# Kernel tuning notes

Measured on AMD Instinct MI355X. Metric: run time of the kernel, lower is better.

Reference implementation:

```python
import math
import jax, jax.numpy as jnp
import numpy as np

D_MODEL = 512
MAX_SEQ = 512
NUM_OUT = 16
H = 1  # num_heads


def _pos_encoding(d_model, seq_len):
    # sinusoidal PE, then flipped along the sequence axis (ReversedPositionalEncoding)
    pos = jnp.arange(seq_len, dtype=jnp.float32)[:, None]
    i = jnp.arange(0, d_model, 2, dtype=jnp.float32)
    ang = pos * jnp.exp(i * (-(math.log(10000.0) / d_model)))  # [S, d/2]
    pe = jnp.stack([jnp.sin(ang), jnp.cos(ang)], axis=-1).reshape(seq_len, d_model)
    return pe[::-1]


def _layernorm(x, w, b, eps=1e-5):
    m = jnp.mean(x, axis=-1, keepdims=True)
    v = jnp.mean(jnp.square(x - m), axis=-1, keepdims=True)
    return (x - m) / jnp.sqrt(v + eps) * w + b


def setup_inputs() -> dict:
    key = jax.random.key(0)
    ks = jax.random.split(key, 8)
    B = 128
    latents = jax.random.normal(ks[0], (B, D_MODEL, MAX_SEQ), dtype=jnp.float32)
    query_mask = jnp.ones((B, NUM_OUT), dtype=jnp.float32)
    query = 0.02 * jax.random.normal(ks[1], (NUM_OUT, D_MODEL), dtype=jnp.float32)
    return {
        "latents": latents,
        "query_mask": query_mask,
        "query": query,
        "ln_lat_w": jnp.ones((D_MODEL,), jnp.float32),
        "ln_lat_b": jnp.zeros((D_MODEL,), jnp.float32),
        "ln_q_w": jnp.ones((D_MODEL,), jnp.float32),
        "ln_q_b": jnp.zeros((D_MODEL,), jnp.float32),
        "Wq": 0.02 * jax.random.normal(ks[2], (D_MODEL, D_MODEL), jnp.float32),
        "bq": jnp.zeros((D_MODEL,), jnp.float32),
        "Wk": 0.02 * jax.random.normal(ks[3], (D_MODEL, D_MODEL), jnp.float32),
        "bk": jnp.zeros((D_MODEL,), jnp.float32),
        "Wv": 0.02 * jax.random.normal(ks[4], (D_MODEL, D_MODEL), jnp.float32),
        "bv": jnp.zeros((D_MODEL,), jnp.float32),
        "Wo": 0.02 * jax.random.normal(ks[5], (1, D_MODEL), jnp.float32),
        "bo": jnp.zeros((1,), jnp.float32),
    }


def reference(latents, query_mask, query, ln_lat_w, ln_lat_b, ln_q_w, ln_q_b,
              Wq, bq, Wk, bk, Wv, bv, Wo, bo):
    B, _, N = latents.shape  # latents: [B, d_model, N]
    scale = math.sqrt(D_MODEL)
    Dh = D_MODEL // H

    # cross-attention mask: query_mask [B,Nq] x all-ones latent mask [B,N]
    mask = jnp.einsum('bq,bk->bqk', query_mask, jnp.ones((B, N), latents.dtype))

    x = jnp.swapaxes(latents, 1, 2) * scale           # [B, N, d]
    x = x + _pos_encoding(D_MODEL, MAX_SEQ)[-N:]      # reversed PE, last N positions
    # dropout is identity in eval mode
    x = _layernorm(x, ln_lat_w, ln_lat_b)

    q = _layernorm(query * scale, ln_q_w, ln_q_b)     # [Nq, d]
    q = jnp.broadcast_to(q[None], (B, NUM_OUT, D_MODEL))

    qh = (q @ Wq.T + bq).reshape(B, NUM_OUT, H, Dh)
    kh = (x @ Wk.T + bk).reshape(B, N, H, Dh)
    vh = (x @ Wv.T + bv).reshape(B, N, H, Dh)

    scores = jnp.einsum('bqhd,bkhd->bhqk', qh, kh) / math.sqrt(Dh)
    scores = jnp.where(mask[:, None] == 0, -1e9, scores)
    attn_weights = jax.nn.softmax(scores, axis=-1)    # [B, H, Nq, N]

    attn = jnp.einsum('bhqk,bkhd->bqhd', attn_weights, vh).reshape(B, NUM_OUT, H * Dh)
    wipe = jnp.all(mask == 0, axis=2, keepdims=True)  # [B, Nq, 1]
    attn = jnp.where(wipe, 0.0, attn)

    logits = attn @ Wo.T + bo                         # [B, Nq, 1]
    return logits, attn_weights
```

## Files before the change

### kernel.cpp

```cpp
#include <hip/hip_runtime.h>
#include <math.h>

#define DM 512
#define NQ 16
#define NG (NQ + 1)

__device__ __forceinline__ float wave_reduce_sum(float v) {
    #pragma unroll
    for (int off = 32; off > 0; off >>= 1) v += __shfl_xor(v, off, 64);
    return v;
}
__device__ __forceinline__ float wave_reduce_max(float v) {
    #pragma unroll
    for (int off = 32; off > 0; off >>= 1) v = fmaxf(v, __shfl_xor(v, off, 64));
    return v;
}

__global__ void k1_setup(const float* __restrict__ Wk, const float* __restrict__ Wv,
                         const float* __restrict__ query,
                         const float* __restrict__ ln_q_w, const float* __restrict__ ln_q_b,
                         float* __restrict__ PET, float* __restrict__ WkT,
                         float* __restrict__ WvT, float* __restrict__ q_ln, int N) {
    __shared__ float tile[64][65];
    int bx = blockIdx.x;
    int lane = threadIdx.x & 63;
    int w = threadIdx.x >> 6;

    if (bx < 128) {
        int ntile = bx & 7, jg = bx >> 3;
        int n = ntile * 64 + lane;
        float p = (float)(N - 1 - n);
        const float c = -logf(10000.f) / (float)DM;
        int jbase = jg * 16 + w * 4;
        #pragma unroll
        for (int u = 0; u < 4; ++u) {
            int j = jbase + u;
            float wj = expf((float)(2 * j) * c);
            float ang = p * wj;
            PET[(size_t)(2 * j) * N + n] = sinf(ang);
            PET[(size_t)(2 * j + 1) * N + n] = cosf(ang);
        }
    } else if (bx < 256) {
        int t = bx - 128;
        const float* W = (t >> 6) ? Wv : Wk;
        float* WT = (t >> 6) ? WvT : WkT;
        int tl = t & 63;
        int te = tl >> 3, td = tl & 7;
        #pragma unroll
        for (int i = 0; i < 16; ++i) {
            int el = w * 16 + i;
            tile[el][lane] = W[(size_t)(te * 64 + el) * DM + td * 64 + lane];
        }
        __syncthreads();
        #pragma unroll
        for (int i = 0; i < 16; ++i) {
            int dl = w * 16 + i;
            WT[(size_t)(td * 64 + dl) * DM + te * 64 + lane] = tile[lane][dl];
        }
    } else {
        const float scale = 22.627416997969522f;
        for (int qi = 0; qi < 4; ++qi) {
            int q = w * 4 + qi;
            float vals[8], s = 0.f, s2 = 0.f;
            #pragma unroll
            for (int i = 0; i < 8; ++i) {
                float x = query[q * DM + i * 64 + lane] * scale;
                vals[i] = x; s += x; s2 += x * x;
            }
            s = wave_reduce_sum(s); s2 = wave_reduce_sum(s2);
            float m = s * (1.f / DM);
            float var = s2 * (1.f / DM) - m * m;
            float rstd = rsqrtf(var + 1e-5f);
            #pragma unroll
            for (int i = 0; i < 8; ++i) {
                int d = i * 64 + lane;
                q_ln[q * DM + d] = (vals[i] - m) * rstd * ln_q_w[d] + ln_q_b[d];
            }
        }
    }
}

__global__ void k2_qh(const float* __restrict__ q_ln, const float* __restrict__ Wq,
                      const float* __restrict__ bq, float* __restrict__ qh) {
    int idx = blockIdx.x * 4 + (threadIdx.x >> 6);
    int lane = threadIdx.x & 63;
    int q = idx >> 9, e = idx & 511;
    const float4* wr = (const float4*)(Wq + (size_t)e * DM);
    const float4* xr = (const float4*)(q_ln + (size_t)q * DM);
    float4 w0 = wr[lane * 2], w1 = wr[lane * 2 + 1];
    float4 x0 = xr[lane * 2], x1 = xr[lane * 2 + 1];
    float s = w0.x * x0.x + w0.y * x0.y + w0.z * x0.z + w0.w * x0.w
            + w1.x * x1.x + w1.y * x1.y + w1.z * x1.z + w1.w * x1.w;
    s = wave_reduce_sum(s);
    if (lane == 0) qh[q * DM + e] = s + bq[e];
}

__global__ void k3_qt(const float* __restrict__ qh, const float* __restrict__ WkT,
                      const float* __restrict__ Wo, const float* __restrict__ WvT,
                      const float* __restrict__ lnw,
                      float* __restrict__ qt, float* __restrict__ A,
                      float* __restrict__ wvout) {
    int idx = blockIdx.x * 4 + (threadIdx.x >> 6);
    int lane = threadIdx.x & 63;
    int g = idx >> 9, d = idx & 511;
    const float4* wr;
    const float4* xr;
    if (g < NQ) {
        wr = (const float4*)(WkT + (size_t)d * DM);
        xr = (const float4*)(qh + (size_t)g * DM);
    } else {
        wr = (const float4*)(WvT + (size_t)d * DM);
        xr = (const float4*)Wo;
    }
    float4 w0 = wr[lane * 2], w1 = wr[lane * 2 + 1];
    float4 x0 = xr[lane * 2], x1 = xr[lane * 2 + 1];
    float s = w0.x * x0.x + w0.y * x0.y + w0.z * x0.z + w0.w * x0.w
            + w1.x * x1.x + w1.y * x1.y + w1.z * x1.z + w1.w * x1.w;
    s = wave_reduce_sum(s);
    if (lane == 0) {
        if (g < NQ) qt[g * DM + d] = s;
        else wvout[d] = s;
        A[g * DM + d] = s * lnw[d];
    }
}

__global__ void k4_pea(const float* __restrict__ A, const float* __restrict__ PET,
                       const float* __restrict__ qt, const float* __restrict__ qh,
                       const float* __restrict__ wv, const float* __restrict__ lnb,
                       const float* __restrict__ bk, const float* __restrict__ Wo,
                       const float* __restrict__ bv,
                       float* __restrict__ peA, float* __restrict__ peS,
                       float* __restrict__ peQ, float* __restrict__ consts, int N) {
    __shared__ float red[4][64];
    int bx = blockIdx.x;
    int lane = threadIdx.x & 63;
    int w = threadIdx.x >> 6;

    if (bx < 152) {
        int g = bx >> 3, ntile = bx & 7;
        int n = ntile * 64 + lane;
        int d0 = w * 128;
        float acc = 0.f;
        if (g < NG) {
            for (int i = 0; i < 128; ++i) {
                int d = d0 + i;
                acc = fmaf(A[(size_t)g * DM + d], PET[(size_t)d * N + n], acc);
            }
        } else if (g == NG) {
            for (int i = 0; i < 128; ++i) acc += PET[(size_t)(d0 + i) * N + n];
        } else {
            for (int i = 0; i < 128; ++i) {
                float v = PET[(size_t)(d0 + i) * N + n];
                acc = fmaf(v, v, acc);
            }
        }
        red[w][lane] = acc;
        __syncthreads();
        if (w != 0) return;
        float tot = red[0][lane] + red[1][lane] + red[2][lane] + red[3][lane];
        if (g < NG) peA[(size_t)g * N + n] = tot;
        else if (g == NG) peS[n] = tot;
        else peQ[n] = tot;
    } else {
        int t = (bx - 152) * 4 + w;
        if (t > NQ) return;
        if (t < NQ) {
            float sa = 0.f, sc = 0.f, qb = 0.f;
            #pragma unroll
            for (int i = 0; i < 8; ++i) {
                int d = i * 64 + lane;
                sa += A[t * DM + d];
                sc = fmaf(qt[t * DM + d], lnb[d], sc);
                qb = fmaf(qh[t * DM + d], bk[d], qb);
            }
            sa = wave_reduce_sum(sa);
            sc = wave_reduce_sum(sc);
            qb = wave_reduce_sum(qb);
            if (lane == 0) { consts[t] = sa; consts[16 + t] = sc + qb; }
        } else {
            float sa = 0.f, cv = 0.f, bvo = 0.f;
            #pragma unroll
            for (int i = 0; i < 8; ++i) {
                int d = i * 64 + lane;
                sa += A[NQ * DM + d];
                cv = fmaf(wv[d], lnb[d], cv);
                bvo = fmaf(Wo[d], bv[d], bvo);
            }
            sa = wave_reduce_sum(sa);
            cv = wave_reduce_sum(cv);
            bvo = wave_reduce_sum(bvo);
            if (lane == 0) { consts[32] = sa; consts[33] = cv + bvo; }
        }
    }
}

__launch_bounds__(256, 4)
__global__ void main_kernel(const float* __restrict__ latents,
                            const float* __restrict__ PET,
                            const float* __restrict__ A,
                            const float* __restrict__ peA,
                            const float* __restrict__ peS,
                            const float* __restrict__ peQ,
                            const float* __restrict__ consts,
                            float* __restrict__ scores,
                            float* __restrict__ vbuf, int N) {
    int b = blockIdx.y;
    int lane = threadIdx.x & 63;
    int wv = threadIdx.x >> 6;
    int n = blockIdx.x * 64 + lane;
    const float scale = 22.627416997969522f;

    int d0 = __builtin_amdgcn_readfirstlane(wv * (DM / 4));
    const float* lat = latents + (size_t)b * DM * N + (size_t)d0 * N + n;
    const float* pet = PET + (size_t)d0 * N + n;

    float acc[NG];
    #pragma unroll
    for (int i = 0; i < NG; ++i) acc[i] = 0.f;
    float S1 = 0.f, S2 = 0.f, Sx = 0.f;

    const int U = 8;
    const int NC = (DM / 4) / U;
    float xb[2][U], pb[2][U];
    #pragma unroll
    for (int u = 0; u < U; ++u) {
        xb[0][u] = __builtin_nontemporal_load(&lat[(size_t)u * N]);
        pb[0][u] = pet[(size_t)u * N];
    }
    int cur = 0;
    for (int c = 0; c < NC; ++c) {
        int nxt = cur ^ 1;
        if (c + 1 < NC) {
            #pragma unroll
            for (int u = 0; u < U; ++u) {
                size_t dd = (size_t)((c + 1) * U + u) * N;
                xb[nxt][u] = __builtin_nontemporal_load(&lat[dd]);
                pb[nxt][u] = pet[dd];
            }
        }
        #pragma unroll
        for (int u = 0; u < U; ++u) {
            float x = xb[cur][u], pe = pb[cur][u];
            S1 += x; S2 = fmaf(x, x, S2); Sx = fmaf(x, pe, Sx);
            int d = d0 + c * U + u;
            #pragma unroll
            for (int q = 0; q < NG; ++q)
                acc[q] = fmaf(A[(size_t)q * DM + d], x, acc[q]);
        }
        cur = nxt;
    }

    __shared__ float red[4][NG + 3][64];
    red[wv][0][lane] = S1;
    red[wv][1][lane] = S2;
    red[wv][2][lane] = Sx;
    #pragma unroll
    for (int i = 0; i < NG; ++i) red[wv][3 + i][lane] = acc[i];
    __syncthreads();
    if (wv != 0) return;

    float tot[NG + 3];
    #pragma unroll
    for (int i = 0; i < NG + 3; ++i)
        tot[i] = red[0][i][lane] + red[1][i][lane] + red[2][i][lane] + red[3][i][lane];

    float s1 = tot[0], s2 = tot[1], sx = tot[2];
    float m = (scale * s1 + peS[n]) * (1.f / DM);
    float ex2 = (scale * scale * s2 + 2.f * scale * sx + peQ[n]) * (1.f / DM);
    float rstd = rsqrtf(ex2 - m * m + 1e-5f);

    float sumAv = consts[32], CvT = consts[33];
    float v = rstd * (scale * tot[3 + NQ] + peA[(size_t)NQ * N + n] - m * sumAv) + CvT;
    vbuf[(size_t)b * N + n] = v;

    const float isd = 0.044194173824159216f;
    #pragma unroll
    for (int q = 0; q < NQ; ++q) {
        float sc = (rstd * (scale * tot[3 + q] + peA[(size_t)q * N + n] - m * consts[q])
                    + consts[16 + q]) * isd;
        scores[((size_t)b * NQ + q) * N + n] = sc;
    }
}

__global__ void softmax_kernel(const float* __restrict__ scores,
                               const float* __restrict__ vbuf,
                               const float* __restrict__ query_mask,
                               const float* __restrict__ bo,
                               float* __restrict__ out_logits,
                               float* __restrict__ out_attn, int N) {
    int r = blockIdx.x * 4 + (threadIdx.x >> 6);
    int b = r >> 4;
    int lane = threadIdx.x & 63;
    float* attn_row = out_attn + (size_t)r * N;
    float qm = query_mask[r];
    if (qm == 0.f) {
        float u = 1.f / (float)N;
        for (int i = 0; i < N / 64; ++i) attn_row[i * 64 + lane] = u;
        if (lane == 0) out_logits[r] = bo[0];
        return;
    }
    const float* srow = scores + (size_t)r * N;
    float sv[8];
    float mx = -1e30f;
    for (int i = 0; i < N / 64; ++i) { sv[i] = srow[i * 64 + lane]; mx = fmaxf(mx, sv[i]); }
    mx = wave_reduce_max(mx);
    float sum = 0.f;
    for (int i = 0; i < N / 64; ++i) { sv[i] = expf(sv[i] - mx); sum += sv[i]; }
    sum = wave_reduce_sum(sum);
    float inv = 1.f / sum;
    const float* vrow = vbuf + (size_t)b * N;
    float lp = 0.f;
    for (int i = 0; i < N / 64; ++i) {
        float w = sv[i] * inv;
        attn_row[i * 64 + lane] = w;
        lp += w * vrow[i * 64 + lane];
    }
    lp = wave_reduce_sum(lp);
    if (lane == 0) out_logits[r] = lp + bo[0];
}

extern "C" void kernel_launch(void* const* d_in, const int* in_sizes, int n_in,
                              void* d_out, int out_size, void* d_ws, size_t ws_size,
                              hipStream_t stream) {
    const float* latents    = (const float*)d_in[0];
    const float* query_mask = (const float*)d_in[1];
    const float* query      = (const float*)d_in[2];
    const float* ln_lat_w   = (const float*)d_in[3];
    const float* ln_lat_b   = (const float*)d_in[4];
    const float* ln_q_w     = (const float*)d_in[5];
    const float* ln_q_b     = (const float*)d_in[6];
    const float* Wq         = (const float*)d_in[7];
    const float* bq         = (const float*)d_in[8];
    const float* Wk         = (const float*)d_in[9];
    const float* bk         = (const float*)d_in[10];
    const float* Wv         = (const float*)d_in[11];
    const float* bv         = (const float*)d_in[12];
    const float* Wo         = (const float*)d_in[13];
    const float* bo         = (const float*)d_in[14];

    int B = in_sizes[1] / NQ;
    int N = in_sizes[0] / (DM * B);

    float* ws = (float*)d_ws;
    size_t off = 0;
    float* PET    = ws + off; off += (size_t)DM * N;
    float* WkT    = ws + off; off += (size_t)DM * DM;
    float* WvT    = ws + off; off += (size_t)DM * DM;
    float* peS    = ws + off; off += N;
    float* peQ    = ws + off; off += N;
    float* q_ln   = ws + off; off += NQ * DM;
    float* qh     = ws + off; off += NQ * DM;
    float* qt     = ws + off; off += NQ * DM;
    float* A      = ws + off; off += NG * DM;
    float* wv     = ws + off; off += DM;
    float* peA    = ws + off; off += (size_t)NG * N;
    float* consts = ws + off; off += 64;
    float* scores = ws + off; off += (size_t)B * NQ * N;
    float* vbuf   = ws + off; off += (size_t)B * N;

    float* out_logits = (float*)d_out;
    float* out_attn   = out_logits + (size_t)B * NQ;

    k1_setup<<<257, 256, 0, stream>>>(Wk, Wv, query, ln_q_w, ln_q_b,
                                      PET, WkT, WvT, q_ln, N);
    k2_qh<<<NQ * DM / 4, 256, 0, stream>>>(q_ln, Wq, bq, qh);
    k3_qt<<<NG * DM / 4, 256, 0, stream>>>(qh, WkT, Wo, WvT, ln_lat_w, qt, A, wv);
    k4_pea<<<157, 256, 0, stream>>>(A, PET, qt, qh, wv, ln_lat_b, bk, Wo, bv,
                                    peA, peS, peQ, consts, N);
    dim3 gmain(N / 64, B);
    main_kernel<<<gmain, 256, 0, stream>>>(latents, PET, A, peA, peS, peQ, consts,
                                           scores, vbuf, N);
    softmax_kernel<<<B * NQ / 4, 256, 0, stream>>>(scores, vbuf, query_mask, bo,
                                                   out_logits, out_attn, N);
}
```

Before: 283.0 us.

## Process two columns per thread with packed FMA and vectorize softmax

The main kernel now has each thread handle two adjacent sequence positions. It uses v_pk_fma_f32 inline asm against a duplicated scalar A coefficient, stored as an extra A2 buffer, to halve the FMA instruction count, and it issues 8-byte vector loads and stores. The grid is halved along N and each wave now covers 128 rows of d. The softmax kernel switches to float4 loads and stores and hardcodes two float4 chunks per lane, which assumes N=512. Each block now streams twice the data, so there are fewer blocks and less parallelism, and register pressure rises.

```diff
diff --git a/kernel.cpp b/kernel.cpp
--- a/kernel.cpp
+++ b/kernel.cpp
@@ -4,6 +4,8 @@
 #define DM 512
 #define NQ 16
 #define NG (NQ + 1)
+
+typedef __attribute__((ext_vector_type(2))) float f32x2;
 
 __device__ __forceinline__ float wave_reduce_sum(float v) {
     #pragma unroll
@@ -99,7 +101,7 @@
                       const float* __restrict__ Wo, const float* __restrict__ WvT,
                       const float* __restrict__ lnw,
                       float* __restrict__ qt, float* __restrict__ A,
-                      float* __restrict__ wvout) {
+                      f32x2* __restrict__ A2, float* __restrict__ wvout) {
     int idx = blockIdx.x * 4 + (threadIdx.x >> 6);
     int lane = threadIdx.x & 63;
     int g = idx >> 9, d = idx & 511;
@@ -120,7 +122,10 @@
     if (lane == 0) {
         if (g < NQ) qt[g * DM + d] = s;
         else wvout[d] = s;
-        A[g * DM + d] = s * lnw[d];
+        float a = s * lnw[d];
+        A[g * DM + d] = a;
+        f32x2 ap; ap.x = a; ap.y = a;
+        A2[g * DM + d] = ap;
     }
 }
 
@@ -197,7 +202,7 @@
 __launch_bounds__(256, 4)
 __global__ void main_kernel(const float* __restrict__ latents,
                             const float* __restrict__ PET,
-                            const float* __restrict__ A,
+                            const unsigned long long* __restrict__ A2,
                             const float* __restrict__ peA,
                             const float* __restrict__ peS,
                             const float* __restrict__ peQ,
@@ -206,26 +211,26 @@
                             float* __restrict__ vbuf, int N) {
     int b = blockIdx.y;
     int lane = threadIdx.x & 63;
-    int wv = threadIdx.x >> 6;
-    int n = blockIdx.x * 64 + lane;
+    int w = threadIdx.x >> 6;
+    int n0 = blockIdx.x * 128 + lane * 2;
     const float scale = 22.627416997969522f;
 
-    int d0 = __builtin_amdgcn_readfirstlane(wv * (DM / 4));
-    const float* lat = latents + (size_t)b * DM * N + (size_t)d0 * N + n;
-    const float* pet = PET + (size_t)d0 * N + n;
-
-    float acc[NG];
-    #pragma unroll
-    for (int i = 0; i < NG; ++i) acc[i] = 0.f;
-    float S1 = 0.f, S2 = 0.f, Sx = 0.f;
-
-    const int U = 8;
-    const int NC = (DM / 4) / U;
-    float xb[2][U], pb[2][U];
+    int d0 = __builtin_amdgcn_readfirstlane(w * 128);
+    const float* latf = latents + (size_t)b * DM * N + (size_t)d0 * N + n0;
+    const float* petf = PET + (size_t)d0 * N + n0;
+
+    f32x2 acc[NG];
+    #pragma unroll
+    for (int i = 0; i < NG; ++i) { acc[i].x = 0.f; acc[i].y = 0.f; }
+    f32x2 S1 = {0.f, 0.f}, S2 = {0.f, 0.f}, Sx = {0.f, 0.f};
+
+    const int U = 4;
+    const int NC = 128 / U;
+    f32x2 xb[2][U], pb[2][U];
     #pragma unroll
     for (int u = 0; u < U; ++u) {
-        xb[0][u] = __builtin_nontemporal_load(&lat[(size_t)u * N]);
-        pb[0][u] = pet[(size_t)u * N];
+        xb[0][u] = __builtin_nontemporal_load((const f32x2*)(latf + (size_t)u * N));
+        pb[0][u] = *(const f32x2*)(petf + (size_t)u * N);
     }
     int cur = 0;
     for (int c = 0; c < NC; ++c) {
@@ -234,51 +239,61 @@
             #pragma unroll
             for (int u = 0; u < U; ++u) {
                 size_t dd = (size_t)((c + 1) * U + u) * N;
-                xb[nxt][u] = __builtin_nontemporal_load(&lat[dd]);
-                pb[nxt][u] = pet[dd];
+                xb[nxt][u] = __builtin_nontemporal_load((const f32x2*)(latf + dd));
+                pb[nxt][u] = *(const f32x2*)(petf + dd);
             }
         }
         #pragma unroll
         for (int u = 0; u < U; ++u) {
-            float x = xb[cur][u], pe = pb[cur][u];
-            S1 += x; S2 = fmaf(x, x, S2); Sx = fmaf(x, pe, Sx);
+            f32x2 x = xb[cur][u], pe = pb[cur][u];
+            S1 += x;
+            S2.x = fmaf(x.x, x.x, S2.x); S2.y = fmaf(x.y, x.y, S2.y);
+            Sx.x = fmaf(x.x, pe.x, Sx.x); Sx.y = fmaf(x.y, pe.y, Sx.y);
             int d = d0 + c * U + u;
             #pragma unroll
-            for (int q = 0; q < NG; ++q)
-                acc[q] = fmaf(A[(size_t)q * DM + d], x, acc[q]);
+            for (int q = 0; q < NG; ++q) {
+                unsigned long long a = A2[(size_t)q * DM + d];
+                asm("v_pk_fma_f32 %0, %1, %2, %0"
+                    : "+v"(acc[q]) : "s"(a), "v"(x));
+            }
         }
         cur = nxt;
     }
 
-    __shared__ float red[4][NG + 3][64];
-    red[wv][0][lane] = S1;
-    red[wv][1][lane] = S2;
-    red[wv][2][lane] = Sx;
-    #pragma unroll
-    for (int i = 0; i < NG; ++i) red[wv][3 + i][lane] = acc[i];
+    __shared__ f32x2 red[4][NG + 3][64];
+    red[w][0][lane] = S1;
+    red[w][1][lane] = S2;
+    red[w][2][lane] = Sx;
+    #pragma unroll
+    for (int i = 0; i < NG; ++i) red[w][3 + i][lane] = acc[i];
     __syncthreads();
-    if (wv != 0) return;
-
-    float tot[NG + 3];
+    if (w != 0) return;
+
+    f32x2 tot[NG + 3];
     #pragma unroll
     for (int i = 0; i < NG + 3; ++i)
         tot[i] = red[0][i][lane] + red[1][i][lane] + red[2][i][lane] + red[3][i][lane];
 
-    float s1 = tot[0], s2 = tot[1], sx = tot[2];
-    float m = (scale * s1 + peS[n]) * (1.f / DM);
-    float ex2 = (scale * scale * s2 + 2.f * scale * sx + peQ[n]) * (1.f / DM);
-    float rstd = rsqrtf(ex2 - m * m + 1e-5f);
+    f32x2 peS2 = *(const f32x2*)(peS + n0);
+    f32x2 peQ2 = *(const f32x2*)(peQ + n0);
+    f32x2 m = (scale * tot[0] + peS2) * (1.f / DM);
+    f32x2 ex2 = (scale * scale * tot[1] + 2.f * scale * tot[2] + peQ2) * (1.f / DM);
+    f32x2 rstd;
+    rstd.x = rsqrtf(ex2.x - m.x * m.x + 1e-5f);
+    rstd.y = rsqrtf(ex2.y - m.y * m.y + 1e-5f);
 
     float sumAv = consts[32], CvT = consts[33];
-    float v = rstd * (scale * tot[3 + NQ] + peA[(size_t)NQ * N + n] - m * sumAv) + CvT;
-    vbuf[(size_t)b * N + n] = v;
+    f32x2 peAv = *(const f32x2*)(peA + (size_t)NQ * N + n0);
+    f32x2 v = rstd * (scale * tot[3 + NQ] + peAv - m * sumAv) + CvT;
+    *(f32x2*)(vbuf + (size_t)b * N + n0) = v;
 
     const float isd = 0.044194173824159216f;
     #pragma unroll
     for (int q = 0; q < NQ; ++q) {
-        float sc = (rstd * (scale * tot[3 + q] + peA[(size_t)q * N + n] - m * consts[q])
+        f32x2 peAq = *(const f32x2*)(peA + (size_t)q * N + n0);
+        f32x2 sc = (rstd * (scale * tot[3 + q] + peAq - m * consts[q])
                     + consts[16 + q]) * isd;
-        scores[((size_t)b * NQ + q) * N + n] = sc;
+        *(f32x2*)(scores + ((size_t)b * NQ + q) * N + n0) = sc;
     }
 }
 
@@ -291,29 +306,41 @@
     int r = blockIdx.x * 4 + (threadIdx.x >> 6);
     int b = r >> 4;
     int lane = threadIdx.x & 63;
-    float* attn_row = out_attn + (size_t)r * N;
+    float4* attn_row = (float4*)(out_attn + (size_t)r * N);
     float qm = query_mask[r];
+    int nv = N / 4;
     if (qm == 0.f) {
         float u = 1.f / (float)N;
-        for (int i = 0; i < N / 64; ++i) attn_row[i * 64 + lane] = u;
+        float4 uv = make_float4(u, u, u, u);
+        for (int i = lane; i < nv; i += 64) attn_row[i] = uv;
         if (lane == 0) out_logits[r] = bo[0];
         return;
     }
-    const float* srow = scores + (size_t)r * N;
-    float sv[8];
-    float mx = -1e30f;
-    for (int i = 0; i < N / 64; ++i) { sv[i] = srow[i * 64 + lane]; mx = fmaxf(mx, sv[i]); }
+    const float4* srow = (const float4*)(scores + (size_t)r * N);
+    float4 sv[2];
+    sv[0] = srow[lane]; sv[1] = srow[64 + lane];
+    float mx = fmaxf(fmaxf(fmaxf(sv[0].x, sv[0].y), fmaxf(sv[0].z, sv[0].w)),
+                     fmaxf(fmaxf(sv[1].x, sv[1].y), fmaxf(sv[1].z, sv[1].w)));
     mx = wave_reduce_max(mx);
     float sum = 0.f;
-    for (int i = 0; i < N / 64; ++i) { sv[i] = expf(sv[i] - mx); sum += sv[i]; }
+    #pragma unroll
+    for (int i = 0; i < 2; ++i) {
+        sv[i].x = expf(sv[i].x - mx); sv[i].y = expf(sv[i].y - mx);
+        sv[i].z = expf(sv[i].z - mx); sv[i].w = expf(sv[i].w - mx);
+        sum += sv[i].x + sv[i].y + sv[i].z + sv[i].w;
+    }
     sum = wave_reduce_sum(sum);
     float inv = 1.f / sum;
-    const float* vrow = vbuf + (size_t)b * N;
+    const float4* vrow = (const float4*)(vbuf + (size_t)b * N);
     float lp = 0.f;
-    for (int i = 0; i < N / 64; ++i) {
-        float w = sv[i] * inv;
-        attn_row[i * 64 + lane] = w;
-        lp += w * vrow[i * 64 + lane];
+    #pragma unroll
+    for (int i = 0; i < 2; ++i) {
+        float4 vv = vrow[i * 64 + lane];
+        float4 wgt;
+        wgt.x = sv[i].x * inv; wgt.y = sv[i].y * inv;
+        wgt.z = sv[i].z * inv; wgt.w = sv[i].w * inv;
+        attn_row[i * 64 + lane] = wgt;
+        lp += wgt.x * vv.x + wgt.y * vv.y + wgt.z * vv.z + wgt.w * vv.w;
     }
     lp = wave_reduce_sum(lp);
     if (lane == 0) out_logits[r] = lp + bo[0];
@@ -352,6 +379,7 @@
     float* qh     = ws + off; off += NQ * DM;
     float* qt     = ws + off; off += NQ * DM;
     float* A      = ws + off; off += NG * DM;
+    float* A2     = ws + off; off += (size_t)NG * DM * 2;
     float* wv     = ws + off; off += DM;
     float* peA    = ws + off; off += (size_t)NG * N;
     float* consts = ws + off; off += 64;
@@ -364,11 +392,14 @@
     k1_setup<<<257, 256, 0, stream>>>(Wk, Wv, query, ln_q_w, ln_q_b,
                                       PET, WkT, WvT, q_ln, N);
     k2_qh<<<NQ * DM / 4, 256, 0, stream>>>(q_ln, Wq, bq, qh);
-    k3_qt<<<NG * DM / 4, 256, 0, stream>>>(qh, WkT, Wo, WvT, ln_lat_w, qt, A, wv);
+    k3_qt<<<NG * DM / 4, 256, 0, stream>>>(qh, WkT, Wo, WvT, ln_lat_w,
+                                           qt, A, (f32x2*)A2, wv);
     k4_pea<<<157, 256, 0, stream>>>(A, PET, qt, qh, wv, ln_lat_b, bk, Wo, bv,
                                     peA, peS, peQ, consts, N);
-    dim3 gmain(N / 64, B);
-    main_kernel<<<gmain, 256, 0, stream>>>(latents, PET, A, peA, peS, peQ, consts,
+    dim3 gmain(N / 128, B);
+    main_kernel<<<gmain, 256, 0, stream>>>(latents, PET,
+                                           (const unsigned long long*)A2,
+                                           peA, peS, peQ, consts,
                                            scores, vbuf, N);
     softmax_kernel<<<B * NQ / 4, 256, 0, stream>>>(scores, vbuf, query_mask, bo,
                                                    out_logits, out_attn, N);
```

Measured after the change: 309.9 us. 9.5% more time.
